# Kernel tuning notes

Measured on AMD Instinct MI355X. Metric: run time of the kernel, lower is better.

## Reference

```python
import jax, jax.numpy as jnp
import numpy as np


def log_g(x):
    # log of g(x) = x + 0.5 for x>=0, sigmoid(x) for x<0
    return jnp.where(x >= 0, jnp.log(jax.nn.relu(x) + 0.5), -jax.nn.softplus(-x))


def setup_inputs() -> dict:
    key = jax.random.key(0)
    k1, k2, k3 = jax.random.split(key, 3)
    bs, seq_len, d_in, H = 4, 4096, 1024, 1024
    scale = 1.0 / np.sqrt(d_in)  # keep pre-activations O(1) so exp() in log-space scan stays finite
    x = jax.random.normal(k1, (bs, seq_len, d_in), dtype=jnp.float32)
    h_0 = jnp.zeros((bs, 1, H), dtype=jnp.float32)
    Wz = jax.random.normal(k2, (H, d_in), dtype=jnp.float32) * scale
    bz = jnp.zeros((H,), dtype=jnp.float32)
    Wh = jax.random.normal(k3, (H, d_in), dtype=jnp.float32) * scale
    bh = jnp.zeros((H,), dtype=jnp.float32)
    return {"x": x, "h_0": h_0, "Wz": Wz, "bz": bz, "Wh": Wh, "bh": bh}


def reference(x, h_0, Wz, bz, Wh, bh):
    bs, seq_len, _ = x.shape
    # gate and candidate pre-activations (two GEMMs)
    k = jnp.einsum("bsd,hd->bsh", x, Wz) + bz          # [bs, S, H]
    log_coeff = -jax.nn.softplus(k)                     # log(1 - z)
    log_z = -jax.nn.softplus(-k)                        # log(z)
    log_tilde_h = log_g(jnp.einsum("bsd,hd->bsh", x, Wh) + bh)
    log_h_0 = log_g(h_0)                                # [bs, 1, H]
    log_value = jnp.concatenate([log_h_0, log_z + log_tilde_h], axis=1)  # [bs, S+1, H]
    # log-space parallel scan: h_t = (1-z_t) h_{t-1} + z_t h~_t
    a_star = jnp.pad(jnp.cumsum(log_coeff, axis=1), ((0, 0), (1, 0), (0, 0)))  # [bs, S+1, H]
    log_h0_plus_b_star = jax.lax.cumlogsumexp(log_value - a_star, axis=1)
    log_prefix = a_star + log_h0_plus_b_star
    return jnp.exp(log_prefix)[:, 1:]                   # [bs, S, H]
```

## Files before the change

kernel.cpp:

```cpp
#include <hip/hip_runtime.h>
#include <cstddef>
#include <cstdint>

#define BSZ   4
#define SEQ   4096
#define DIN   1024
#define HDIM  1024
#define MTOT  (BSZ * SEQ)
#define NELE  ((size_t)MTOT * HDIM)
#define NX    ((size_t)MTOT * DIN)
#define NW    ((size_t)HDIM * DIN)
#define NCH   128
#define CL    (SEQ / NCH)

#define X4 (NX / 4)
#define W4 (NW / 4)

#define GBM 256
#define GBN 128
#define GBK 64
#define NKT (DIN / GBK)

using bf16x8 = __attribute__((ext_vector_type(8))) __bf16;
using f32x4  = __attribute__((ext_vector_type(4))) float;

__device__ __forceinline__ float bf2f(unsigned int u16bits) {
    union { unsigned int i; float f; } v;
    v.i = u16bits << 16;
    return v.f;
}
__device__ __forceinline__ unsigned int pk2(float a, float b) {
    union { float f; unsigned int i; } ua, ub; ua.f = a; ub.f = b;
    return ((ua.i + 0x8000u) >> 16) | ((ub.i + 0x8000u) & 0xffff0000u);
}

__device__ __forceinline__ void gload16(const void* g, void* l) {
    __builtin_amdgcn_global_load_lds(
        (const __attribute__((address_space(1))) unsigned int*)g,
        (__attribute__((address_space(3))) unsigned int*)l, 16, 0, 0);
}

__global__ __launch_bounds__(256) void cvt_bf16(
    const float* __restrict__ x, const float* __restrict__ wz,
    const float* __restrict__ wh, unsigned short* __restrict__ xb,
    unsigned short* __restrict__ zb, unsigned short* __restrict__ hb)
{
    const size_t i = (size_t)blockIdx.x * 256 + threadIdx.x;
    const float4* s; uint2* d; size_t off;
    if (i < X4)           { s = (const float4*)x;  d = (uint2*)xb; off = i; }
    else if (i < X4 + W4) { s = (const float4*)wz; d = (uint2*)zb; off = i - X4; }
    else                  { s = (const float4*)wh; d = (uint2*)hb; off = i - X4 - W4; }
    const float4 v = s[off];
    uint2 r;
    r.x = pk2(v.x, v.y);
    r.y = pk2(v.z, v.w);
    d[off] = r;
}

#define SBAR  __builtin_amdgcn_sched_barrier(0)
#define PRIO1 __builtin_amdgcn_s_setprio(1)
#define PRIO0 __builtin_amdgcn_s_setprio(0)

#define MFMA1(acc, va, vb) \
    acc = __builtin_amdgcn_mfma_f32_16x16x32_bf16(va, vb, acc, 0, 0, 0)

#define MFMA_PAIR(P, AV, S)                                                    \
    _Pragma("unroll")                                                          \
    for (int i_ = 0; i_ < 2; ++i_) {                                           \
        _Pragma("unroll")                                                      \
        for (int nt_ = 0; nt_ < 2; ++nt_) {                                    \
            MFMA1(accz[2*(P)+i_][nt_], AV[i_][0], Bz[S][nt_][0]);              \
            MFMA1(acch[2*(P)+i_][nt_], AV[i_][0], Bh[S][nt_][0]);              \
            MFMA1(accz[2*(P)+i_][nt_], AV[i_][1], Bz[S][nt_][1]);              \
            MFMA1(acch[2*(P)+i_][nt_], AV[i_][1], Bh[S][nt_][1]);              \
        }                                                                      \
    }

#define READ_A(AV, MTP, B)                                                     \
    AV[0][0] = *(const bf16x8*)((B) + aBase + (2*(MTP)+0)*2048 + k0o);         \
    AV[0][1] = *(const bf16x8*)((B) + aBase + (2*(MTP)+0)*2048 + k1o);         \
    AV[1][0] = *(const bf16x8*)((B) + aBase + (2*(MTP)+1)*2048 + k0o);         \
    AV[1][1] = *(const bf16x8*)((B) + aBase + (2*(MTP)+1)*2048 + k1o);

#define READ_B_HALF(SS, NT, B)                                                 \
    Bz[SS][NT][0] = *(const bf16x8*)((B) + zBase + (NT)*2048 + k0o);           \
    Bz[SS][NT][1] = *(const bf16x8*)((B) + zBase + (NT)*2048 + k1o);           \
    Bh[SS][NT][0] = *(const bf16x8*)((B) + hBase + (NT)*2048 + k0o);           \
    Bh[SS][NT][1] = *(const bf16x8*)((B) + hBase + (NT)*2048 + k1o);

#define STAGE8(BN, KO)                                                         \
    gload16(gA + (KO),          (BN) + ldsA);                                  \
    gload16(gA + (KO) + 16384,  (BN) + ldsA + 512);                            \
    gload16(gA + (KO) + 32768,  (BN) + ldsA + 1024);                           \
    gload16(gA + (KO) + 49152,  (BN) + ldsA + 1536);                           \
    gload16(gZ + (KO),          (BN) + ldsZ);                                  \
    gload16(gZ + (KO) + 16384,  (BN) + ldsZ + 512);                            \
    gload16(gH + (KO),          (BN) + ldsH);                                  \
    gload16(gH + (KO) + 16384,  (BN) + ldsH + 512);

#define TILE(KT, S)                                                            \
    {                                                                          \
        const int ktv = (KT);                                                  \
        const char*     bcc = (const char*)&smem[S][0];                        \
        unsigned short* bn  = &smem[(S) ^ 1][0];                               \
        const char*     bnc = (const char*)bn;                                 \
        const bool pf = (ktv + 1 < NKT);                                       \
        const size_t ko = (size_t)(ktv + 1) * 128;                             \
                                                                       \
        if (pf) { STAGE8(bn, ko) }                                             \
        READ_A(A1, 1, bcc)                                                     \
        PRIO1; MFMA_PAIR(0, A0, S) PRIO0; SBAR;                                \
                                                                       \
        READ_A(A0, 2, bcc)                                                     \
        PRIO1; MFMA_PAIR(1, A1, S) PRIO0; SBAR;                                \
                                                                       \
        READ_A(A1, 3, bcc)                                                     \
        PRIO1; MFMA_PAIR(2, A0, S) PRIO0; SBAR;                                \
                \
        if (pf) {                                                              \
            asm volatile("s_waitcnt vmcnt(0)" ::: "memory");                   \
            __builtin_amdgcn_s_barrier();                                      \
            READ_B_HALF((S) ^ 1, 0, bnc)                                       \
            READ_A(A0, 0, bnc)                                                 \
        }                                                                      \
        PRIO1; MFMA_PAIR(3, A1, S) PRIO0; SBAR;                                \
        if (pf) { READ_B_HALF((S) ^ 1, 1, bnc) }                               \
    }

__global__ __launch_bounds__(512, 1) void gemm_act_8ph(
    const unsigned short* __restrict__ xb, const unsigned short* __restrict__ zb,
    const unsigned short* __restrict__ hb, const float* __restrict__ bz,
    const float* __restrict__ bh, unsigned int* __restrict__ ab,
    float* __restrict__ carryA, float* __restrict__ carryB)
{
    __shared__ unsigned short smem[2][32768];

    const int tid  = threadIdx.x;
    const int wid  = tid >> 6;
    const int lane = tid & 63;
    const int lm   = lane & 15;
    const int q    = lane >> 4;
    const int wr   = wid >> 2;
    const int wc   = wid & 3;

    const int bid = blockIdx.x;
    const int swz = (bid & 7) * 64 + (bid >> 3);
    const int ty  = swz >> 3;
    const int tx  = swz & 7;
    const int m0  = ty * GBM;
    const int n0  = tx * GBN;

    const int l8   = lane >> 3;
    const int sl   = lane & 7;
    const int scol = 16 * (sl ^ l8);
    const char* gA = (const char*)xb + ((size_t)(m0 + wid * 32 + l8) * DIN) * 2 + scol;
    const char* gZ = (const char*)zb + ((size_t)(n0 + wid * 16 + l8) * DIN) * 2 + scol;
    const char* gH = (const char*)hb + ((size_t)(n0 + wid * 16 + l8) * DIN) * 2 + scol;
    const int ldsA = wid * 2048;
    const int ldsZ = 16384 + wid * 1024;
    const int ldsH = 24576 + wid * 1024;

    const int sw  = (lm & 7) << 4;
    const int k0o = (q * 16) ^ sw;
    const int k1o = (64 + q * 16) ^ sw;
    const int aBase = (wr * 128 + lm) * 128;
    const int zBase = 32768 + (wc * 32 + lm) * 128;
    const int hBase = 49152 + (wc * 32 + lm) * 128;

    f32x4 accz[8][2], acch[8][2];
#pragma unroll
    for (int mt = 0; mt < 8; ++mt)
#pragma unroll
        for (int nt = 0; nt < 2; ++nt) {
            accz[mt][nt] = (f32x4){0.f, 0.f, 0.f, 0.f};
            acch[mt][nt] = (f32x4){0.f, 0.f, 0.f, 0.f};
        }

    bf16x8 A0[2][2], A1[2][2];
    bf16x8 Bz[2][2][2], Bh[2][2][2];

    {
        unsigned short* b0 = &smem[0][0];
        const char*     b0c = (const char*)b0;
        STAGE8(b0, 0)
        asm volatile("s_waitcnt vmcnt(0)" ::: "memory");
        __builtin_amdgcn_s_barrier();
        READ_B_HALF(0, 0, b0c)
        READ_B_HALF(0, 1, b0c)
        READ_A(A0, 0, b0c)
    }

    for (int kt = 0; kt < NKT; kt += 2) {
        TILE(kt, 0)
        TILE(kt + 1, 1)
    }

    const int bi  = m0 >> 12;
    const int cb0 = ((m0 & 4095) >> 5) + wr * 4;

#pragma unroll
    for (int nt = 0; nt < 2; ++nt) {
        const int col = n0 + wc * 32 + nt * 16 + lm;
        const float bzv = bz[col];
        const float bhv = bh[col];
#pragma unroll
        for (int pr = 0; pr < 4; ++pr) {
            float CA = 1.f, CB = 0.f;
#pragma unroll
            for (int mi = 0; mi < 2; ++mi) {
                const int mt   = pr * 2 + mi;
                const int row0 = m0 + wr * 128 + mt * 16 + q * 4;
                float A = 1.f, B = 0.f;
#pragma unroll
                for (int r = 0; r < 4; ++r) {
                    const float kpre = accz[mt][nt][r] + bzv;
                    const float hpre = acch[mt][nt][r] + bhv;
                    const float ez   = __expf(-kpre);
                    const float zv   = 1.0f / (1.0f + ez);
                    const float avv  = ez * zv;
                    const float g    = (hpre >= 0.f) ? (hpre + 0.5f)
                                                     : (1.0f / (1.0f + __expf(-hpre)));
                    const float bv   = zv * g;
                    ab[(size_t)(row0 + r) * HDIM + col] = pk2(avv, bv);
                    A = avv * A;
                    B = fmaf(avv, B, bv);
                }
                float A2 = __shfl_xor(A, 16, 64);
                float B2 = __shfl_xor(B, 16, 64);
                B = (q & 1) ? fmaf(A, B2, B) : fmaf(A2, B, B2);
                A = A * A2;
                A2 = __shfl_xor(A, 32, 64);
                B2 = __shfl_xor(B, 32, 64);
                B = (q & 2) ? fmaf(A, B2, B) : fmaf(A2, B, B2);
                A = A * A2;
                CB = fmaf(A, CB, B);
                CA = A * CA;
            }
            if (q == 0) {
                const int cseq = cb0 + pr;
                const size_t ci = ((size_t)(cseq * BSZ + bi)) * HDIM + col;
                carryA[ci] = CA;
                carryB[ci] = CB;
            }
        }
    }
}

__global__ __launch_bounds__(256) void scan_phaseB(
    const float* __restrict__ h0, const float* __restrict__ carryA,
    const float* __restrict__ carryB, float* __restrict__ hin)
{
    const int h  = blockIdx.x * 256 + threadIdx.x;
    const int bi = blockIdx.y;
    const float v = h0[(size_t)bi * HDIM + h];
    float hr = (v >= 0.0f) ? (v + 0.5f) : (1.0f / (1.0f + __expf(-v)));
    for (int c0 = 0; c0 < NCH; c0 += 8) {
        float a[8], b[8];
#pragma unroll
        for (int j = 0; j < 8; ++j) {
            const size_t ci = ((size_t)(c0 + j) * BSZ + bi) * HDIM + h;
            a[j] = carryA[ci];
            b[j] = carryB[ci];
        }
#pragma unroll
        for (int j = 0; j < 8; ++j) {
            const size_t ci = ((size_t)(c0 + j) * BSZ + bi) * HDIM + h;
            hin[ci] = hr;
            hr = fmaf(a[j], hr, b[j]);
        }
    }
}

__global__ __launch_bounds__(256) void scan_phaseC(
    const unsigned int* __restrict__ ab, const float* __restrict__ hin,
    float* __restrict__ out)
{
    const int c  = blockIdx.x;
    const int bi = blockIdx.y;
    const int h  = (blockIdx.z * 256 + threadIdx.x) * 2;
    size_t idx = ((size_t)bi * SEQ + (size_t)c * CL) * HDIM + h;
    const size_t ci = ((size_t)c * BSZ + bi) * HDIM + h;
    float2 hr = *(const float2*)&hin[ci];
    uint2 v = *(const uint2*)&ab[idx];
#pragma unroll 4
    for (int t = 0; t < CL; ++t) {
        uint2 vn;
        if (t + 1 < CL) vn = *(const uint2*)&ab[idx + HDIM];
        hr.x = fmaf(bf2f(v.x & 0xffffu), hr.x, bf2f(v.x >> 16));
        hr.y = fmaf(bf2f(v.y & 0xffffu), hr.y, bf2f(v.y >> 16));
        *(float2*)&out[idx] = hr;
        v = vn;
        idx += HDIM;
    }
}

extern "C" void kernel_launch(void* const* d_in, const int* in_sizes, int n_in,
                              void* d_out, int out_size, void* d_ws, size_t ws_size,
                              hipStream_t stream)
{
    const float* x  = (const float*)d_in[0];
    const float* h0 = (const float*)d_in[1];
    const float* Wz = (const float*)d_in[2];
    const float* bz = (const float*)d_in[3];
    const float* Wh = (const float*)d_in[4];
    const float* bh = (const float*)d_in[5];
    float* out = (float*)d_out;

    unsigned int*   ab  = (unsigned int*)d_ws;
    unsigned short* xbf = (unsigned short*)(ab + NELE);
    unsigned short* zbf = xbf + NX;
    unsigned short* hbf = zbf + NW;
    float* carryA = (float*)(hbf + NW);
    float* carryB = carryA + (size_t)NCH * BSZ * HDIM;
    float* hin    = carryB + (size_t)NCH * BSZ * HDIM;

    const int cvtBlocks = (int)((X4 + 2 * W4) / 256);
    cvt_bf16<<<cvtBlocks, 256, 0, stream>>>(x, Wz, Wh, xbf, zbf, hbf);

    dim3 gGrid((MTOT / GBM) * (HDIM / GBN));
    gemm_act_8ph<<<gGrid, 512, 0, stream>>>(xbf, zbf, hbf, bz, bh, ab, carryA, carryB);

    dim3 bGrid(HDIM / 256, BSZ);
    scan_phaseB<<<bGrid, 256, 0, stream>>>(h0, carryA, carryB, hin);

    dim3 cGrid(NCH, BSZ, 2);
    scan_phaseC<<<cGrid, 256, 0, stream>>>(ab, hin, out);
}
```

Before: 231.3 us.

## Restructure GEMM K-loop into barrier-synchronized phases with split A/B prefetch

Reorganizes the double-buffered GEMM main loop into four phases, each separated by workgroup barriers and explicit lgkmcnt waits. Global-to-LDS prefetch of the B tiles (Wz/Wh) is issued in phase 0 and the A tile (x) in phase 1, which spreads the loads across the tile. It uses a partial vmcnt(4) wait so the next B fragments can be read before the A loads finish. This aims for a more regular interleave of LDS reads, global loads and MFMAs across waves, in the style of 8-wave ping-pong schedules. The cost is many extra s_barriers per K-tile, which can stall waves and reduce overlap.

```diff
diff --git a/kernel.cpp b/kernel.cpp
--- a/kernel.cpp
+++ b/kernel.cpp
@@ -58,8 +58,10 @@
 }
 
 #define SBAR  __builtin_amdgcn_sched_barrier(0)
+#define BARR  __builtin_amdgcn_s_barrier()
 #define PRIO1 __builtin_amdgcn_s_setprio(1)
 #define PRIO0 __builtin_amdgcn_s_setprio(0)
+#define LGKM0 asm volatile("s_waitcnt lgkmcnt(0)" ::: "memory")
 
 #define MFMA1(acc, va, vb) \
     acc = __builtin_amdgcn_mfma_f32_16x16x32_bf16(va, vb, acc, 0, 0, 0)
@@ -88,15 +90,16 @@
     Bh[SS][NT][0] = *(const bf16x8*)((B) + hBase + (NT)*2048 + k0o);           \
     Bh[SS][NT][1] = *(const bf16x8*)((B) + hBase + (NT)*2048 + k1o);
 
-#define STAGE8(BN, KO)                                                         \
-    gload16(gA + (KO),          (BN) + ldsA);                                  \
-    gload16(gA + (KO) + 16384,  (BN) + ldsA + 512);                            \
-    gload16(gA + (KO) + 32768,  (BN) + ldsA + 1024);                           \
-    gload16(gA + (KO) + 49152,  (BN) + ldsA + 1536);                           \
+#define STAGE_B(BN, KO)                                                        \
     gload16(gZ + (KO),          (BN) + ldsZ);                                  \
     gload16(gZ + (KO) + 16384,  (BN) + ldsZ + 512);                            \
     gload16(gH + (KO),          (BN) + ldsH);                                  \
     gload16(gH + (KO) + 16384,  (BN) + ldsH + 512);
+#define STAGE_A(BN, KO)                                                        \
+    gload16(gA + (KO),          (BN) + ldsA);                                  \
+    gload16(gA + (KO) + 16384,  (BN) + ldsA + 512);                            \
+    gload16(gA + (KO) + 32768,  (BN) + ldsA + 1024);                           \
+    gload16(gA + (KO) + 49152,  (BN) + ldsA + 1536);
 
 #define TILE(KT, S)                                                            \
     {                                                                          \
@@ -106,25 +109,28 @@
         const char*     bnc = (const char*)bn;                                 \
         const bool pf = (ktv + 1 < NKT);                                       \
         const size_t ko = (size_t)(ktv + 1) * 128;                             \
-                                                                       \
-        if (pf) { STAGE8(bn, ko) }                                             \
+                                             \
+        READ_A(A0, 0, bcc)                                                     \
+        if (pf) { STAGE_B(bn, ko) }                                            \
+        BARR; LGKM0; SBAR;                                                     \
+        PRIO1; MFMA_PAIR(0, A0, S) PRIO0; BARR;                                \
+                                             \
         READ_A(A1, 1, bcc)                                                     \
-        PRIO1; MFMA_PAIR(0, A0, S) PRIO0; SBAR;                                \
-                                                                       \
+        if (pf) { STAGE_A(bn, ko) }                                            \
+        BARR; LGKM0; SBAR;                                                     \
+        PRIO1; MFMA_PAIR(1, A1, S) PRIO0; BARR;                                \
+                                                           \
         READ_A(A0, 2, bcc)                                                     \
-        PRIO1; MFMA_PAIR(1, A1, S) PRIO0; SBAR;                                \
-                                                                       \
+        BARR; LGKM0; SBAR;                                                     \
+        PRIO1; MFMA_PAIR(2, A0, S) PRIO0; BARR;                                \
+              \
         READ_A(A1, 3, bcc)                                                     \
-        PRIO1; MFMA_PAIR(2, A0, S) PRIO0; SBAR;                                \
-                \
-        if (pf) {                                                              \
-            asm volatile("s_waitcnt vmcnt(0)" ::: "memory");                   \
-            __builtin_amdgcn_s_barrier();                                      \
-            READ_B_HALF((S) ^ 1, 0, bnc)                                       \
-            READ_A(A0, 0, bnc)                                                 \
-        }                                                                      \
-        PRIO1; MFMA_PAIR(3, A1, S) PRIO0; SBAR;                                \
-        if (pf) { READ_B_HALF((S) ^ 1, 1, bnc) }                               \
+        if (pf) { asm volatile("s_waitcnt vmcnt(4)" ::: "memory"); }           \
+        BARR;                                        \
+        if (pf) { READ_B_HALF((S) ^ 1, 0, bnc) READ_B_HALF((S) ^ 1, 1, bnc) }  \
+        PRIO1; MFMA_PAIR(3, A1, S) PRIO0;          \
+        if (pf) { asm volatile("s_waitcnt vmcnt(0)" ::: "memory"); }           \
+        BARR;                                        \
     }
 
 __global__ __launch_bounds__(512, 1) void gemm_act_8ph(
@@ -182,12 +188,12 @@
     {
         unsigned short* b0 = &smem[0][0];
         const char*     b0c = (const char*)b0;
-        STAGE8(b0, 0)
+        STAGE_B(b0, 0)
+        STAGE_A(b0, 0)
         asm volatile("s_waitcnt vmcnt(0)" ::: "memory");
-        __builtin_amdgcn_s_barrier();
+        BARR;
         READ_B_HALF(0, 0, b0c)
         READ_B_HALF(0, 1, b0c)
-        READ_A(A0, 0, b0c)
     }
 
     for (int kt = 0; kt < NKT; kt += 2) {
```

New measurement: 239.9 us. 1.04x slower.
